# Kernel tuning notes

Hardware: AMD Instinct MI355X
Metric: run time of the kernel (lower is better)

The kernel has to match this reference:

```python
import jax, jax.numpy as jnp
import numpy as np

H, W = 101, 31
HEADS, DH, FREQ = 8, 64, 64
C_DIM = 256
INNER = HEADS * DH
EPS = 1e-5


def _conv2d(x, w, b):
    # x: (B, Cin, H, W), w: (Cout, Cin, 3, 3) -> SAME padding, stride 1
    y = jax.lax.conv_general_dilated(x, w, (1, 1), 'SAME',
                                     dimension_numbers=('NCHW', 'OIHW', 'NCHW'))
    return y + b[None, :, None, None]


def setup_inputs() -> dict:
    key = jax.random.key(0)
    ks = jax.random.split(key, 8)
    B = 32
    N = H * W  # 3131
    s = 0.02
    x = jax.random.normal(ks[0], (B, N, C_DIM), jnp.float32)
    conv_fx_w = jax.random.normal(ks[1], (INNER, C_DIM, 3, 3), jnp.float32) * s
    conv_fx_b = jnp.zeros((INNER,), jnp.float32)
    conv_x_w = jax.random.normal(ks[2], (INNER, C_DIM, 3, 3), jnp.float32) * s
    conv_x_b = jnp.zeros((INNER,), jnp.float32)
    gate_w = jax.random.normal(ks[3], (FREQ, DH), jnp.float32) * s  # nn.Linear weight (out,in)
    gate_b = jnp.zeros((FREQ,), jnp.float32)
    temperature = jnp.full((1, HEADS, 1, 1), 0.5, jnp.float32)
    ln_gamma = jnp.ones((FREQ, DH), jnp.float32)
    ln_beta = jnp.zeros((FREQ, DH), jnp.float32)
    mlp_w = jax.random.normal(ks[4], (DH, DH), jnp.float32) * s
    out_w = jax.random.normal(ks[5], (C_DIM, INNER), jnp.float32) * s
    out_b = jnp.zeros((C_DIM,), jnp.float32)
    # fixed (non-trainable) spectral basis, L2-normalized per row like F.normalize(dim=-1)
    inver = jax.random.normal(ks[6], (N, FREQ), jnp.float32)
    inver = inver / jnp.linalg.norm(inver, axis=-1, keepdims=True)
    return dict(x=x, conv_fx_w=conv_fx_w, conv_fx_b=conv_fx_b, conv_x_w=conv_x_w,
                conv_x_b=conv_x_b, gate_w=gate_w, gate_b=gate_b,
                temperature=temperature, ln_gamma=ln_gamma, ln_beta=ln_beta,
                mlp_w=mlp_w, out_w=out_w, out_b=out_b, inver=inver)


def reference(x, conv_fx_w, conv_fx_b, conv_x_w, conv_x_b, gate_w, gate_b,
              temperature, ln_gamma, ln_beta, mlp_w, out_w, out_b, inver):
    B, N, C = x.shape
    xi = x.reshape(B, H, W, C).transpose(0, 3, 1, 2)  # (B, C, H, W)

    def proj(w, b):
        y = _conv2d(xi, w, b)                                  # (B, inner, H, W)
        return y.transpose(0, 2, 3, 1).reshape(B, N, HEADS, DH).transpose(0, 2, 1, 3)  # (B,h,N,d)

    fx_mid = proj(conv_fx_w, conv_fx_b)
    x_mid = proj(conv_x_w, conv_x_b)

    temp = jnp.clip(temperature, 0.1, 5.0)                      # (1,h,1,1)
    logits = jnp.einsum('bhnc,gc->bhng', x_mid, gate_w) + gate_b
    gate = jax.nn.softmax(logits / temp, axis=-1)               # (B,h,N,g)
    eigens = gate * inver[None, None]                           # (B,h,N,g)

    spec = jnp.einsum('bhnc,bhng->bhgc', fx_mid, eigens)        # (B,h,g,c)
    # LayerNorm over the trailing (g, c) axes jointly
    mu = spec.mean(axis=(-2, -1), keepdims=True)
    var = spec.var(axis=(-2, -1), keepdims=True)
    spec = (spec - mu) * jax.lax.rsqrt(var + EPS) * ln_gamma + ln_beta

    out_spec = jnp.einsum('bhgi,io->bhgo', spec, mlp_w)
    out_x = jnp.einsum('bhgc,bhng->bhnc', out_spec, eigens)     # (B,h,N,c)
    out_x = out_x.transpose(0, 2, 1, 3).reshape(B, N, HEADS * DH)
    return jnp.einsum('bnd,cd->bnc', out_x, out_w) + out_b      # to_out (dropout is identity)
```

## Files before the change

kernel.cpp:

```cpp
#include <hip/hip_runtime.h>
#include <hip/hip_bf16.h>
#include <stdint.h>

#define HH 101
#define WW 31
#define NN 3131
#define NPAD 3136
#define BB 32
#define NH 8
#define CDIM 256
#define GG 64
#define HP 103
#define WP 33

typedef __attribute__((ext_vector_type(8))) short bf16x8;
typedef __attribute__((ext_vector_type(4))) float f32x4;
typedef __attribute__((ext_vector_type(4))) unsigned short ushort4_t;
typedef __attribute__((ext_vector_type(8))) unsigned short ushort8_t;
typedef __attribute__((ext_vector_type(4))) float float4_t;

static __device__ __forceinline__ unsigned short f2bf(float f) {
  union { float f; uint32_t u; } v; v.f = f;
  uint32_t u = v.u;
  return (unsigned short)((u + 0x7fffu + ((u >> 16) & 1u)) >> 16);
}
static __device__ __forceinline__ float bf2f(unsigned short h) {
  union { uint32_t u; float f; } v; v.u = ((uint32_t)h) << 16;
  return v.f;
}
static __device__ __forceinline__ void gload_lds16(const void* g, void* l) {
  __builtin_amdgcn_global_load_lds((const __attribute__((address_space(1))) void*)g,
                                   (__attribute__((address_space(3))) void*)l, 16, 0, 0);
}
static __device__ __forceinline__ int xcd_swz(int bid, int nwg) {
  int q = nwg >> 3, r = nwg & 7;
  int xcd = bid & 7, pos = bid >> 3;
  int base = (xcd < r) ? xcd * (q + 1) : r * (q + 1) + (xcd - r) * q;
  return base + pos;
}

__global__ void k_pad(const float* __restrict__ x, unsigned short* __restrict__ xpad, int b0) {
  const int xx = blockIdx.x, yy = blockIdx.y, b = blockIdx.z;
  const int t = threadIdx.x;
  ushort4_t o; o.x = 0; o.y = 0; o.z = 0; o.w = 0;
  if (yy >= 1 && yy <= HH && xx >= 1 && xx <= WW) {
    const int n = (yy - 1) * WW + (xx - 1);
    const float4_t v = *(const float4_t*)(x + (((int64_t)(b0 + b) * NN + n) * CDIM + t * 4));
    o.x = f2bf(v.x); o.y = f2bf(v.y); o.z = f2bf(v.z); o.w = f2bf(v.w);
  }
  *(ushort4_t*)(xpad + (((int64_t)b * HP + yy) * WP + xx) * CDIM + t * 4) = o;
}

__global__ void k_wpack(const float* __restrict__ fxw, const float* __restrict__ xw,
                        const float* __restrict__ fxb, const float* __restrict__ xb,
                        const float* __restrict__ gw,
                        unsigned short* __restrict__ Wb, float* __restrict__ bias,
                        unsigned short* __restrict__ gwb) {
  int tid = blockIdx.x * blockDim.x + threadIdx.x;
  const int total = 9 * 1024 * 256;
  if (tid < total) {
    int cin = tid & 255; int rest = tid >> 8; int co = rest & 1023; int t = rest >> 10;
    float v = (co < 512) ? fxw[(int64_t)co * 2304 + cin * 9 + t]
                         : xw[(int64_t)(co - 512) * 2304 + cin * 9 + t];
    Wb[tid] = f2bf(v);
  }
  if (tid < 1024) bias[tid] = (tid < 512) ? fxb[tid] : xb[tid - 512];
  if (tid < 4096) gwb[tid] = f2bf(gw[tid]);
}

__global__ void k_pprep(const float* __restrict__ mlp, const float* __restrict__ outw,
                        unsigned short* __restrict__ Pt) {
  int h = blockIdx.x >> 6, i = blockIdx.x & 63, co = threadIdx.x;
  float a = 0.f;
  for (int c = 0; c < 64; ++c) a += mlp[i * 64 + c] * outw[(int64_t)co * 512 + h * 64 + c];
  Pt[((int64_t)h * 256 + co) * 64 + i] = f2bf(a);
}

__global__ void k_padzero(unsigned short* __restrict__ fxT, unsigned short* __restrict__ xmid,
                          int CB) {
  int tid = blockIdx.x * blockDim.x + threadIdx.x;
  if (tid >= CB * 2560) return;
  {
    int j = tid % 5; int rc = tid / 5;
    fxT[(int64_t)rc * NPAD + NN + j] = 0;
  }
  {
    int d = tid & 63; int rest = tid >> 6;
    int j = rest % 5; int bh = rest / 5;
    xmid[((int64_t)bh * NPAD + NN + j) * 64 + d] = 0;
  }
}

__launch_bounds__(512, 2)
__global__ void k_conv8(const unsigned short* __restrict__ xpad,
                        const unsigned short* __restrict__ Wb,
                        const float* __restrict__ bias,
                        unsigned short* __restrict__ fxT,
                        unsigned short* __restrict__ xmid) {
  extern __shared__ unsigned short lds[];
  const int swz = xcd_swz(blockIdx.x, gridDim.x);
  const int r   = swz % 52;
  const int b   = swz / 52;
  const int bx  = r & 3;
  const int mt  = r >> 2;
  const int tid = threadIdx.x, wid = tid >> 6, lane = tid & 63;
  const int wm = wid >> 2, wn = wid & 3;
  const int arow = lane & 15, col16 = lane >> 4;
  const int n00 = mt * 256, co00 = bx * 256;

  const int srow = wid * 16 + (lane >> 2);
  const int tc   = ((lane & 3) ^ ((lane >> 3) & 3)) * 8;
  int na0 = n00 + srow;        if (na0 >= NN) na0 = NN - 1;
  int na1 = n00 + srow + 128;  if (na1 >= NN) na1 = NN - 1;
  const int y0 = na0 / WW, x0v = na0 % WW;
  const int y1 = na1 / WW, x1v = na1 % WW;
  const unsigned short* aS0 = xpad + ((int64_t)(b * HP + y0) * WP + x0v) * CDIM + tc;
  const unsigned short* aS1 = xpad + ((int64_t)(b * HP + y1) * WP + x1v) * CDIM + tc;
  const unsigned short* bS0 = Wb + (int64_t)(co00 + srow) * CDIM + tc;
  const unsigned short* bS1 = Wb + (int64_t)(co00 + srow + 128) * CDIM + tc;

  const int rdsz = (col16 ^ ((arow >> 1) & 3)) * 8;

  f32x4 acc[8][4] = {};

#define STAGE_A(s, kk, aoffv)                                        \
  { unsigned short* d = lds + (s) * 32768 + (kk) * 8192 + wid * 512; \
    gload_lds16(aS0 + (aoffv) + (kk) * 32, d);                       \
    gload_lds16(aS1 + (aoffv) + (kk) * 32, d + 4096); }
#define STAGE_B(s, kk, boffv)                                                \
  { unsigned short* d = lds + (s) * 32768 + 16384 + (kk) * 8192 + wid * 512; \
    gload_lds16(bS0 + (boffv) + (kk) * 32, d);                               \
    gload_lds16(bS1 + (boffv) + (kk) * 32, d + 4096); }
#define KOFF(ks, aoffv, boffv)                              \
  { const int tap = (ks) >> 2;                              \
    const int dy = (tap >= 6) + (tap >= 3);                 \
    const int dx = tap - dy * 3;                            \
    const int cb = ((ks) & 3) << 6;                         \
    aoffv = (dy * WP + dx) * CDIM + cb;                     \
    boffv = tap * 262144 + cb; }

  int aoff0, boff0;
  KOFF(0, aoff0, boff0);
  STAGE_A(0, 0, aoff0); STAGE_B(0, 0, boff0);
  STAGE_A(0, 1, aoff0); STAGE_B(0, 1, boff0);
  asm volatile("s_waitcnt vmcnt(4)" ::: "memory");
  __builtin_amdgcn_s_barrier();
  asm volatile("" ::: "memory");

#define MFMA_PAIR(n0i, n1i)                                                              \
  __builtin_amdgcn_s_setprio(1);                                                        \
  _Pragma("unroll")                                                                      \
  for (int mf = 0; mf < 8; ++mf) {                                                       \
    acc[mf][n0i] = __builtin_amdgcn_mfma_f32_16x16x32_bf16(av[mf], bv0, acc[mf][n0i], 0, 0, 0); \
    acc[mf][n1i] = __builtin_amdgcn_mfma_f32_16x16x32_bf16(av[mf], bv1, acc[mf][n1i], 0, 0, 0); \
  }                                                                                      \
  __builtin_amdgcn_s_setprio(0);
#define BAR_PRE()                                              \
  __builtin_amdgcn_s_barrier();                                \
  asm volatile("s_waitcnt lgkmcnt(0)" ::: "memory");           \
  __builtin_amdgcn_sched_barrier(0);
#define BAR_POST()                                             \
  asm volatile("" ::: "memory");                               \
  __builtin_amdgcn_s_barrier();                                \
  asm volatile("" ::: "memory");

  #pragma unroll 1
  for (int t = 0; t < 36; ++t) {
    const int cur = t & 1, nxt = cur ^ 1;
    const int tn = (t < 35) ? t + 1 : 35;
    int aoffn, boffn;
    KOFF(tn, aoffn, boffn);
    unsigned short* sA0 = lds + cur * 32768;
    unsigned short* sB0 = sA0 + 16384;
    bf16x8 av[8], bv0, bv1;

    #pragma unroll
    for (int mf = 0; mf < 8; ++mf)
      av[mf] = *(const bf16x8*)(sA0 + (wm * 128 + mf * 16 + arow) * 32 + rdsz);
    bv0 = *(const bf16x8*)(sB0 + (wn * 64 + 0 + arow) * 32 + rdsz);
    bv1 = *(const bf16x8*)(sB0 + (wn * 64 + 16 + arow) * 32 + rdsz);
    STAGE_A(nxt, 0, aoffn);
    BAR_PRE();
    MFMA_PAIR(0, 1);
    BAR_POST();

    bv0 = *(const bf16x8*)(sB0 + (wn * 64 + 32 + arow) * 32 + rdsz);
    bv1 = *(const bf16x8*)(sB0 + (wn * 64 + 48 + arow) * 32 + rdsz);
    STAGE_B(nxt, 0, boffn);
    asm volatile("s_waitcnt vmcnt(4)" ::: "memory");
    BAR_PRE();
    MFMA_PAIR(2, 3);
    BAR_POST();

    #pragma unroll
    for (int mf = 0; mf < 8; ++mf)
      av[mf] = *(const bf16x8*)(sA0 + 8192 + (wm * 128 + mf * 16 + arow) * 32 + rdsz);
    bv0 = *(const bf16x8*)(sB0 + 8192 + (wn * 64 + 0 + arow) * 32 + rdsz);
    bv1 = *(const bf16x8*)(sB0 + 8192 + (wn * 64 + 16 + arow) * 32 + rdsz);
    STAGE_A(nxt, 1, aoffn);
    BAR_PRE();
    MFMA_PAIR(0, 1);
    BAR_POST();

    bv0 = *(const bf16x8*)(sB0 + 8192 + (wn * 64 + 32 + arow) * 32 + rdsz);
    bv1 = *(const bf16x8*)(sB0 + 8192 + (wn * 64 + 48 + arow) * 32 + rdsz);
    STAGE_B(nxt, 1, boffn);
    asm volatile("s_waitcnt vmcnt(4)" ::: "memory");
    BAR_PRE();
    MFMA_PAIR(2, 3);
    BAR_POST();
  }

  asm volatile("s_waitcnt vmcnt(0)" ::: "memory");

  const int rowoff = col16 * 4;
  #pragma unroll
  for (int mf = 0; mf < 8; ++mf) {
    const int nr = n00 + wm * 128 + mf * 16 + rowoff;
    #pragma unroll
    for (int nf = 0; nf < 4; ++nf) {
      const int co = co00 + wn * 64 + nf * 16 + arow;
      const float bvs = bias[co];
      const float v0 = acc[mf][nf][0] + bvs;
      const float v1 = acc[mf][nf][1] + bvs;
      const float v2 = acc[mf][nf][2] + bvs;
      const float v3 = acc[mf][nf][3] + bvs;
      if (bx < 2) {
        const int h = co >> 6, c = co & 63;
        unsigned short* dst = fxT + ((int64_t)((b * NH + h) * 64 + c)) * NPAD + nr;
        if (nr + 3 < NN) {
          ushort4_t o; o.x = f2bf(v0); o.y = f2bf(v1); o.z = f2bf(v2); o.w = f2bf(v3);
          *(ushort4_t*)dst = o;
        } else {
          if (nr + 0 < NN) dst[0] = f2bf(v0);
          if (nr + 1 < NN) dst[1] = f2bf(v1);
          if (nr + 2 < NN) dst[2] = f2bf(v2);
          if (nr + 3 < NN) dst[3] = f2bf(v3);
        }
      } else {
        const int h = (co >> 6) & 7, d = co & 63;
        unsigned short* dst = xmid + ((int64_t)(b * NH + h) * NPAD + nr) * 64 + d;
        if (nr + 0 < NN) dst[0] = f2bf(v0);
        if (nr + 1 < NN) dst[64] = f2bf(v1);
        if (nr + 2 < NN) dst[128] = f2bf(v2);
        if (nr + 3 < NN) dst[192] = f2bf(v3);
      }
    }
  }
#undef STAGE_A
#undef STAGE_B
#undef KOFF
#undef MFMA_PAIR
#undef BAR_PRE
#undef BAR_POST
}

__global__ void k_eig(const unsigned short* __restrict__ xmid,
                      const unsigned short* __restrict__ gwb,
                      const float* __restrict__ gateb,
                      const float* __restrict__ temperature,
                      const float* __restrict__ inver,
                      unsigned short* __restrict__ eigT,
                      unsigned short* __restrict__ eigN) {
  __shared__ unsigned short egN[64 * 72];
  __shared__ unsigned short egT[64 * 72];
  const int nt = blockIdx.x, h = blockIdx.y, b = blockIdx.z;
  const int tid = threadIdx.x;
  const int w = tid >> 6, lane = tid & 63;
  const int n0 = nt * 64 + w * 16;
  const int bh = b * NH + h;
  float tv = temperature[h];
  tv = fminf(fmaxf(tv, 0.1f), 5.0f);
  const float itemp = 1.0f / tv;
  const int arow = lane & 15;
  const int koff = (lane >> 4) * 8;
  const unsigned short* aptr = xmid + ((int64_t)bh * NPAD + (n0 + arow)) * 64 + koff;
  bf16x8 a0 = *(const bf16x8*)(aptr);
  bf16x8 a1 = *(const bf16x8*)(aptr + 32);
  f32x4 acc[4] = {};
  #pragma unroll
  for (int ng = 0; ng < 4; ++ng) {
    const unsigned short* bptr = gwb + (ng * 16 + arow) * 64 + koff;
    bf16x8 b0 = *(const bf16x8*)(bptr);
    bf16x8 b1 = *(const bf16x8*)(bptr + 32);
    acc[ng] = __builtin_amdgcn_mfma_f32_16x16x32_bf16(a0, b0, acc[ng], 0, 0, 0);
    acc[ng] = __builtin_amdgcn_mfma_f32_16x16x32_bf16(a1, b1, acc[ng], 0, 0, 0);
  }
  #pragma unroll
  for (int r = 0; r < 4; ++r) {
    const int nl = w * 16 + ((lane >> 4) << 2) + r;
    const int n = nt * 64 + nl;
    float vals[4];
    #pragma unroll
    for (int ng = 0; ng < 4; ++ng) vals[ng] = (acc[ng][r] + gateb[ng * 16 + arow]) * itemp;
    float mx = fmaxf(fmaxf(vals[0], vals[1]), fmaxf(vals[2], vals[3]));
    #pragma unroll
    for (int s = 1; s < 16; s <<= 1) mx = fmaxf(mx, __shfl_xor(mx, s));
    float ex[4]; float sum = 0.f;
    #pragma unroll
    for (int ng = 0; ng < 4; ++ng) { ex[ng] = __expf(vals[ng] - mx); sum += ex[ng]; }
    #pragma unroll
    for (int s = 1; s < 16; s <<= 1) sum += __shfl_xor(sum, s);
    const float inv = 1.0f / sum;
    const bool valid = (n < NN);
    #pragma unroll
    for (int ng = 0; ng < 4; ++ng) {
      const int g = ng * 16 + arow;
      float iv = valid ? inver[(int64_t)n * GG + g] : 0.f;
      unsigned short u = valid ? f2bf(ex[ng] * inv * iv) : (unsigned short)0;
      egN[nl * 72 + g] = u;
      egT[g * 72 + nl] = u;
    }
  }
  __syncthreads();
  const int row = tid >> 2, c0 = (tid & 3) << 4;
  {
    ushort8_t v0 = *(ushort8_t*)&egN[row * 72 + c0];
    ushort8_t v1 = *(ushort8_t*)&egN[row * 72 + c0 + 8];
    unsigned short* dst = eigN + ((int64_t)bh * NPAD + nt * 64 + row) * 64 + c0;
    *(ushort8_t*)dst = v0; *(ushort8_t*)(dst + 8) = v1;
  }
  {
    ushort8_t v0 = *(ushort8_t*)&egT[row * 72 + c0];
    ushort8_t v1 = *(ushort8_t*)&egT[row * 72 + c0 + 8];
    unsigned short* dst = eigT + ((int64_t)(bh * 64 + row)) * NPAD + nt * 64 + c0;
    *(ushort8_t*)dst = v0; *(ushort8_t*)(dst + 8) = v1;
  }
}

__launch_bounds__(256, 1)
__global__ void k_specln(const unsigned short* __restrict__ eigT,
                         const unsigned short* __restrict__ fxT,
                         const float* __restrict__ gamma, const float* __restrict__ beta,
                         const unsigned short* __restrict__ Pt,
                         unsigned short* __restrict__ m2t) {
  extern __shared__ char sm[];
  float* sacc = (float*)sm;
  unsigned short* specb = (unsigned short*)(sm + 66560);
  float* red = (float*)(sm + 74752);
  unsigned short* mstrip = (unsigned short*)(sm + 74784);
  const int bhl = blockIdx.x;
  const int h = bhl & 7, bl = bhl >> 3;
  const int tid = threadIdx.x, w = tid >> 6, lane = tid & 63;
  const int arow = lane & 15, col16 = lane >> 4;
  const int koff = col16 * 8;
  const unsigned short* eb = eigT + (int64_t)bhl * 64 * NPAD;
  const unsigned short* fb = fxT + (int64_t)bhl * 64 * NPAD;

  const int ks0 = (98 * w) >> 2, ks1 = (98 * (w + 1)) >> 2;
  f32x4 acc[4][4] = {};
  for (int ks = ks0; ks < ks1; ++ks) {
    const int k0 = ks * 32 + koff;
    bf16x8 av[4], bv[4];
    #pragma unroll
    for (int mg = 0; mg < 4; ++mg) av[mg] = *(const bf16x8*)(eb + (int64_t)(mg * 16 + arow) * NPAD + k0);
    #pragma unroll
    for (int ng = 0; ng < 4; ++ng) bv[ng] = *(const bf16x8*)(fb + (int64_t)(ng * 16 + arow) * NPAD + k0);
    #pragma unroll
    for (int mg = 0; mg < 4; ++mg)
      #pragma unroll
      for (int ng = 0; ng < 4; ++ng)
        acc[mg][ng] = __builtin_amdgcn_mfma_f32_16x16x32_bf16(av[mg], bv[ng], acc[mg][ng], 0, 0, 0);
  }
  float* pw = sacc + w * (64 * 65);
  #pragma unroll
  for (int mg = 0; mg < 4; ++mg)
    #pragma unroll
    for (int ng = 0; ng < 4; ++ng)
      #pragma unroll
      for (int r = 0; r < 4; ++r)
        pw[(mg * 16 + col16 * 4 + r) * 65 + ng * 16 + arow] = acc[mg][ng][r];
  __syncthreads();

  float vloc[16];
  float lsum = 0.f, lsq = 0.f;
  #pragma unroll
  for (int idx = 0; idx < 16; ++idx) {
    const int e = tid + idx * 256;
    const int g = e >> 6, c = e & 63;
    float v = sacc[g * 65 + c] + sacc[4160 + g * 65 + c] +
              sacc[8320 + g * 65 + c] + sacc[12480 + g * 65 + c];
    vloc[idx] = v; lsum += v; lsq += v * v;
  }
  #pragma unroll
  for (int s = 1; s < 64; s <<= 1) { lsum += __shfl_xor(lsum, s); lsq += __shfl_xor(lsq, s); }
  if (lane == 0) { red[w] = lsum; red[4 + w] = lsq; }
  __syncthreads();
  const float tsum = red[0] + red[1] + red[2] + red[3];
  const float tsq = red[4] + red[5] + red[6] + red[7];
  const float mu = tsum * (1.0f / 4096.0f);
  const float var = tsq * (1.0f / 4096.0f) - mu * mu;
  const float rs = rsqrtf(var + 1e-5f);
  #pragma unroll
  for (int idx = 0; idx < 16; ++idx) {
    const int e = tid + idx * 256;
    const int g = e >> 6, c = e & 63;
    float sv = (vloc[idx] - mu) * rs * gamma[e] + beta[e];
    specb[g * 64 + ((((c >> 3) ^ (g & 7))) << 3) + (c & 7)] = f2bf(sv);
  }
  __syncthreads();

  f32x4 a2[4][4] = {};
  const unsigned short* pth = Pt + ((int64_t)h * 256 + w * 64) * 64;
  #pragma unroll
  for (int kk = 0; kk < 2; ++kk) {
    const int i0 = kk * 32 + koff;
    const int i8 = (i0 >> 3);
    bf16x8 av2[4], bv2[4];
    #pragma unroll
    for (int mg = 0; mg < 4; ++mg) {
      const int g = mg * 16 + arow;
      av2[mg] = *(const bf16x8*)(specb + g * 64 + ((i8 ^ (g & 7)) << 3));
    }
    #pragma unroll
    for (int ng = 0; ng < 4; ++ng)
      bv2[ng] = *(const bf16x8*)(pth + (ng * 16 + arow) * 64 + i0);
    #pragma unroll
    for (int mg = 0; mg < 4; ++mg)
      #pragma unroll
      for (int ng = 0; ng < 4; ++ng)
        a2[mg][ng] = __builtin_amdgcn_mfma_f32_16x16x32_bf16(av2[mg], bv2[ng], a2[mg][ng], 0, 0, 0);
  }
  unsigned short* ms = mstrip + w * (64 * 72);
  #pragma unroll
  for (int mg = 0; mg < 4; ++mg)
    #pragma unroll
    for (int ng = 0; ng < 4; ++ng)
      #pragma unroll
      for (int r = 0; r < 4; ++r)
        ms[(ng * 16 + arow) * 72 + mg * 16 + col16 * 4 + r] = f2bf(a2[mg][ng][r]);
  __syncthreads();
  #pragma unroll
  for (int e0 = 0; e0 < 8; ++e0) {
    const int e = lane + e0 * 64;
    const int row = e >> 3, g8 = e & 7;
    ushort8_t v = *(ushort8_t*)&ms[row * 72 + g8 * 8];
    *(ushort8_t*)(m2t + ((int64_t)(bl * 256 + w * 64 + row)) * 512 + h * 64 + g8 * 8) = v;
  }
}

__launch_bounds__(256)
__global__ void k_out(const unsigned short* __restrict__ eigN,
                      const unsigned short* __restrict__ m2t,
                      const float* __restrict__ outb,
                      float* __restrict__ out, int b0) {
  const int swz = xcd_swz(blockIdx.x, gridDim.x);
  const int ct = swz & 1;
  const int mt = (swz >> 1) % 25;
  const int b  = swz / 50;
  const int w = threadIdx.x >> 6, lane = threadIdx.x & 63;
  const int wm = w >> 1, wn = w & 1;
  const int arow = lane & 15, koff = (lane >> 4) * 8;
  const int co0 = ct * 128 + wn * 64;
  const int n0 = mt * 128 + wm * 64;
  f32x4 acc[4][4] = {};
  const unsigned short* ebase = eigN + (int64_t)b * NH * NPAD * 64;
  const unsigned short* mbase = m2t + (int64_t)b * 256 * 512;
  for (int ks = 0; ks < 16; ++ks) {
    const int hh = ks >> 1;
    const int g0 = (ks & 1) * 32 + koff;
    bf16x8 av[4], bv[4];
    #pragma unroll
    for (int mg = 0; mg < 4; ++mg) {
      int n = n0 + mg * 16 + arow;
      if (n > NPAD - 1) n = NPAD - 1;
      av[mg] = *(const bf16x8*)(ebase + ((int64_t)hh * NPAD + n) * 64 + g0);
    }
    #pragma unroll
    for (int ng = 0; ng < 4; ++ng)
      bv[ng] = *(const bf16x8*)(mbase + (int64_t)(co0 + ng * 16 + arow) * 512 + ks * 32 + koff);
    #pragma unroll
    for (int mg = 0; mg < 4; ++mg)
      #pragma unroll
      for (int ng = 0; ng < 4; ++ng)
        acc[mg][ng] = __builtin_amdgcn_mfma_f32_16x16x32_bf16(av[mg], bv[ng], acc[mg][ng], 0, 0, 0);
  }
  #pragma unroll
  for (int mg = 0; mg < 4; ++mg) {
    const int nr = n0 + mg * 16 + ((lane >> 4) << 2);
    #pragma unroll
    for (int ng = 0; ng < 4; ++ng) {
      const int co = co0 + ng * 16 + arow;
      const float bv = outb[co];
      #pragma unroll
      for (int r = 0; r < 4; ++r) {
        if (nr + r < NN)
          out[((int64_t)(b0 + b) * NN + nr + r) * 256 + co] = acc[mg][ng][r] + bv;
      }
    }
  }
}

extern "C" void kernel_launch(void* const* d_in, const int* in_sizes, int n_in,
                              void* d_out, int out_size, void* d_ws, size_t ws_size,
                              hipStream_t stream) {
  const float* x     = (const float*)d_in[0];
  const float* fxw   = (const float*)d_in[1];
  const float* fxb   = (const float*)d_in[2];
  const float* xw    = (const float*)d_in[3];
  const float* xb    = (const float*)d_in[4];
  const float* gw    = (const float*)d_in[5];
  const float* gb    = (const float*)d_in[6];
  const float* temp  = (const float*)d_in[7];
  const float* gamma = (const float*)d_in[8];
  const float* beta  = (const float*)d_in[9];
  const float* mlp   = (const float*)d_in[10];
  const float* outw  = (const float*)d_in[11];
  const float* outb  = (const float*)d_in[12];
  const float* inver = (const float*)d_in[13];
  float* out = (float*)d_out;
  char* ws = (char*)d_ws;
  (void)in_sizes; (void)n_in; (void)out_size;

  hipFuncSetAttribute(reinterpret_cast<const void*>(k_conv8),
                      hipFuncAttributeMaxDynamicSharedMemorySize, 131072);
  hipFuncSetAttribute(reinterpret_cast<const void*>(k_specln),
                      hipFuncAttributeMaxDynamicSharedMemorySize, 131072);

  int CB = 1;
  {
    const int cands[6] = {32, 16, 8, 4, 2, 1};
    for (int i = 0; i < 6; ++i) {
      unsigned long long need = 4993024ull + (unsigned long long)cands[i] * 14847488ull;
      if (need <= (unsigned long long)ws_size) { CB = cands[i]; break; }
    }
  }

  unsigned short* Wb   = (unsigned short*)(ws + 0);
  float*          bias = (float*)(ws + 4718592);
  unsigned short* gwb  = (unsigned short*)(ws + 4722688);
  unsigned short* Pt   = (unsigned short*)(ws + 4730880);
  const size_t F0      = 4993024;
  const size_t szXpad  = (size_t)CB * 1740288;
  const size_t szM2t   = (size_t)CB * 262144;
  const size_t szBig   = (size_t)CB * 3211264;
  unsigned short* xpad = (unsigned short*)(ws + F0);
  unsigned short* m2t  = (unsigned short*)(ws + F0 + szXpad);
  unsigned short* fxT  = (unsigned short*)(ws + F0 + szXpad + szM2t);
  unsigned short* xmid = (unsigned short*)(ws + F0 + szXpad + szM2t + szBig);
  unsigned short* eigT = (unsigned short*)(ws + F0 + szXpad + szM2t + 2 * szBig);
  unsigned short* eigN = (unsigned short*)(ws + F0 + szXpad + szM2t + 3 * szBig);

  k_wpack<<<dim3(9216), dim3(256), 0, stream>>>(fxw, xw, fxb, xb, gw, Wb, bias, gwb);
  k_pprep<<<dim3(512), dim3(256), 0, stream>>>(mlp, outw, Pt);

  for (int b0 = 0; b0 < BB; b0 += CB) {
    k_pad<<<dim3(WP, HP, CB), dim3(64), 0, stream>>>(x, xpad, b0);
    k_padzero<<<dim3(CB * 10), dim3(256), 0, stream>>>(fxT, xmid, CB);
    k_conv8<<<dim3(52 * CB), dim3(512), 131072, stream>>>(xpad, Wb, bias, fxT, xmid);
    k_eig<<<dim3(49, 8, CB), dim3(256), 0, stream>>>(xmid, gwb, gb, temp, inver, eigT, eigN);
    k_specln<<<dim3(CB * 8), dim3(256), 111648, stream>>>(eigT, fxT, gamma, beta, Pt, m2t);
    k_out<<<dim3(50 * CB), dim3(256), 0, stream>>>(eigN, m2t, outb, out, b0);
  }
}
```

Measured before the change: 905.6 us.

## Reshape conv wave tile to 64x128 and software-pipeline LDS fragment reads

```diff
diff --git a/kernel.cpp b/kernel.cpp
--- a/kernel.cpp
+++ b/kernel.cpp
@@ -104,7 +104,7 @@
   const int bx  = r & 3;
   const int mt  = r >> 2;
   const int tid = threadIdx.x, wid = tid >> 6, lane = tid & 63;
-  const int wm = wid >> 2, wn = wid & 3;
+  const int wm = wid & 3, wn = wid >> 2;
   const int arow = lane & 15, col16 = lane >> 4;
   const int n00 = mt * 256, co00 = bx * 256;
 
@@ -121,7 +121,8 @@
 
   const int rdsz = (col16 ^ ((arow >> 1) & 3)) * 8;
 
-  f32x4 acc[8][4] = {};
+  f32x4 acc[4][8] = {};
+  bf16x8 a0[4], a1[4], b03[4], b47[4];
 
 #define STAGE_A(s, kk, aoffv)                                        \
   { unsigned short* d = lds + (s) * 32768 + (kk) * 8192 + wid * 512; \
@@ -138,6 +139,22 @@
     const int cb = ((ks) & 3) << 6;                         \
     aoffv = (dy * WP + dx) * CDIM + cb;                     \
     boffv = tap * 262144 + cb; }
+#define RD_A(dst, s, kk, mf)                                                             \
+  dst = *(const bf16x8*)(lds + (s) * 32768 + (kk) * 8192 +                               \
+                         (wm * 64 + (mf) * 16 + arow) * 32 + rdsz);
+#define RD_B(dst, s, kk, nf)                                                             \
+  dst = *(const bf16x8*)(lds + (s) * 32768 + 16384 + (kk) * 8192 +                       \
+                         (wn * 128 + (nf) * 16 + arow) * 32 + rdsz);
+#define MFMA16(aset, bset, nbase)                                                        \
+  __builtin_amdgcn_s_setprio(1);                                                         \
+  _Pragma("unroll")                                                                      \
+  for (int mf = 0; mf < 4; ++mf) {                                                       \
+    _Pragma("unroll")                                                                    \
+    for (int nf = 0; nf < 4; ++nf)                                                       \
+      acc[mf][(nbase) + nf] =                                                            \
+        __builtin_amdgcn_mfma_f32_16x16x32_bf16(aset[mf], bset[nf], acc[mf][(nbase) + nf], 0, 0, 0); \
+  }                                                                                      \
+  __builtin_amdgcn_s_setprio(0);
 
   int aoff0, boff0;
   KOFF(0, aoff0, boff0);
@@ -146,23 +163,10 @@
   asm volatile("s_waitcnt vmcnt(4)" ::: "memory");
   __builtin_amdgcn_s_barrier();
   asm volatile("" ::: "memory");
-
-#define MFMA_PAIR(n0i, n1i)                                                              \
-  __builtin_amdgcn_s_setprio(1);                                                        \
-  _Pragma("unroll")                                                                      \
-  for (int mf = 0; mf < 8; ++mf) {                                                       \
-    acc[mf][n0i] = __builtin_amdgcn_mfma_f32_16x16x32_bf16(av[mf], bv0, acc[mf][n0i], 0, 0, 0); \
-    acc[mf][n1i] = __builtin_amdgcn_mfma_f32_16x16x32_bf16(av[mf], bv1, acc[mf][n1i], 0, 0, 0); \
-  }                                                                                      \
-  __builtin_amdgcn_s_setprio(0);
-#define BAR_PRE()                                              \
-  __builtin_amdgcn_s_barrier();                                \
-  asm volatile("s_waitcnt lgkmcnt(0)" ::: "memory");           \
-  __builtin_amdgcn_sched_barrier(0);
-#define BAR_POST()                                             \
-  asm volatile("" ::: "memory");                               \
-  __builtin_amdgcn_s_barrier();                                \
-  asm volatile("" ::: "memory");
+  #pragma unroll
+  for (int i = 0; i < 4; ++i) { RD_A(a0[i], 0, 0, i); }
+  #pragma unroll
+  for (int i = 0; i < 4; ++i) { RD_B(b03[i], 0, 0, i); }
 
   #pragma unroll 1
   for (int t = 0; t < 36; ++t) {
@@ -170,56 +174,55 @@
     const int tn = (t < 35) ? t + 1 : 35;
     int aoffn, boffn;
     KOFF(tn, aoffn, boffn);
-    unsigned short* sA0 = lds + cur * 32768;
-    unsigned short* sB0 = sA0 + 16384;
-    bf16x8 av[8], bv0, bv1;
-
-    #pragma unroll
-    for (int mf = 0; mf < 8; ++mf)
-      av[mf] = *(const bf16x8*)(sA0 + (wm * 128 + mf * 16 + arow) * 32 + rdsz);
-    bv0 = *(const bf16x8*)(sB0 + (wn * 64 + 0 + arow) * 32 + rdsz);
-    bv1 = *(const bf16x8*)(sB0 + (wn * 64 + 16 + arow) * 32 + rdsz);
+
+    #pragma unroll
+    for (int i = 0; i < 4; ++i) { RD_B(b47[i], cur, 0, 4 + i); }
     STAGE_A(nxt, 0, aoffn);
-    BAR_PRE();
-    MFMA_PAIR(0, 1);
-    BAR_POST();
-
-    bv0 = *(const bf16x8*)(sB0 + (wn * 64 + 32 + arow) * 32 + rdsz);
-    bv1 = *(const bf16x8*)(sB0 + (wn * 64 + 48 + arow) * 32 + rdsz);
+    asm volatile("s_waitcnt lgkmcnt(4)" ::: "memory");
+    __builtin_amdgcn_sched_barrier(0);
+    MFMA16(a0, b03, 0);
+
     STAGE_B(nxt, 0, boffn);
     asm volatile("s_waitcnt vmcnt(4)" ::: "memory");
-    BAR_PRE();
-    MFMA_PAIR(2, 3);
-    BAR_POST();
-
-    #pragma unroll
-    for (int mf = 0; mf < 8; ++mf)
-      av[mf] = *(const bf16x8*)(sA0 + 8192 + (wm * 128 + mf * 16 + arow) * 32 + rdsz);
-    bv0 = *(const bf16x8*)(sB0 + 8192 + (wn * 64 + 0 + arow) * 32 + rdsz);
-    bv1 = *(const bf16x8*)(sB0 + 8192 + (wn * 64 + 16 + arow) * 32 + rdsz);
+    __builtin_amdgcn_s_barrier();
+    asm volatile("" ::: "memory");
+    #pragma unroll
+    for (int i = 0; i < 4; ++i) { RD_A(a1[i], cur, 1, i); }
+    #pragma unroll
+    for (int i = 0; i < 4; ++i) { RD_B(b03[i], cur, 1, i); }
+    asm volatile("s_waitcnt lgkmcnt(8)" ::: "memory");
+    __builtin_amdgcn_sched_barrier(0);
+    MFMA16(a0, b47, 4);
+
+    #pragma unroll
+    for (int i = 0; i < 4; ++i) { RD_B(b47[i], cur, 1, 4 + i); }
     STAGE_A(nxt, 1, aoffn);
-    BAR_PRE();
-    MFMA_PAIR(0, 1);
-    BAR_POST();
-
-    bv0 = *(const bf16x8*)(sB0 + 8192 + (wn * 64 + 32 + arow) * 32 + rdsz);
-    bv1 = *(const bf16x8*)(sB0 + 8192 + (wn * 64 + 48 + arow) * 32 + rdsz);
+    asm volatile("s_waitcnt lgkmcnt(4)" ::: "memory");
+    __builtin_amdgcn_sched_barrier(0);
+    MFMA16(a1, b03, 0);
+
     STAGE_B(nxt, 1, boffn);
     asm volatile("s_waitcnt vmcnt(4)" ::: "memory");
-    BAR_PRE();
-    MFMA_PAIR(2, 3);
-    BAR_POST();
-  }
-
-  asm volatile("s_waitcnt vmcnt(0)" ::: "memory");
+    __builtin_amdgcn_s_barrier();
+    asm volatile("" ::: "memory");
+    #pragma unroll
+    for (int i = 0; i < 4; ++i) { RD_A(a0[i], nxt, 0, i); }
+    #pragma unroll
+    for (int i = 0; i < 4; ++i) { RD_B(b03[i], nxt, 0, i); }
+    asm volatile("s_waitcnt lgkmcnt(8)" ::: "memory");
+    __builtin_amdgcn_sched_barrier(0);
+    MFMA16(a1, b47, 4);
+  }
+
+  asm volatile("s_waitcnt vmcnt(0) lgkmcnt(0)" ::: "memory");
 
   const int rowoff = col16 * 4;
   #pragma unroll
-  for (int mf = 0; mf < 8; ++mf) {
-    const int nr = n00 + wm * 128 + mf * 16 + rowoff;
-    #pragma unroll
-    for (int nf = 0; nf < 4; ++nf) {
-      const int co = co00 + wn * 64 + nf * 16 + arow;
+  for (int mf = 0; mf < 4; ++mf) {
+    const int nr = n00 + wm * 64 + mf * 16 + rowoff;
+    #pragma unroll
+    for (int nf = 0; nf < 8; ++nf) {
+      const int co = co00 + wn * 128 + nf * 16 + arow;
       const float bvs = bias[co];
       const float v0 = acc[mf][nf][0] + bvs;
       const float v1 = acc[mf][nf][1] + bvs;
@@ -250,9 +253,9 @@
 #undef STAGE_A
 #undef STAGE_B
 #undef KOFF
-#undef MFMA_PAIR
-#undef BAR_PRE
-#undef BAR_POST
+#undef RD_A
+#undef RD_B
+#undef MFMA16
 }
 
 __global__ void k_eig(const unsigned short* __restrict__ xmid,
```

Measured after the change: 884.9 us. -2.3%, faster.
